# Kernel tuning notes

Hardware: AMD Instinct MI355X
Metric: run time of the kernel (lower is better)

The kernel has to match this reference:

```python
import jax, jax.numpy as jnp
import numpy as np

EPS = 1e-5
GROUPS = 32
K = 7  # correlation kernel size (min(7, 14))


def group_norm(x, w, b):
    B, C, H, W = x.shape
    xg = x.reshape(B, GROUPS, C // GROUPS, H, W)
    m = xg.mean(axis=(2, 3, 4), keepdims=True)
    v = xg.var(axis=(2, 3, 4), keepdims=True)
    xg = (xg - m) * jax.lax.rsqrt(v + EPS)
    return xg.reshape(B, C, H, W) * w[None, :, None, None] + b[None, :, None, None]


def conv1x1(x, w):  # w: [O, C]
    return jnp.einsum('bchw,oc->bohw', x, w)


def setup_inputs() -> dict:
    key = jax.random.key(0)
    ks = jax.random.split(key, 16)
    C, CC = 256, 64
    d = {}
    d['template_feat'] = jax.random.normal(ks[0], (32, C, 14, 14), jnp.float32)
    d['search_feat'] = jax.random.normal(ks[1], (32, C, 64, 64), jnp.float32)
    s1 = 1.0 / np.sqrt(C)
    d['w_t'] = jax.random.normal(ks[2], (CC, C), jnp.float32) * s1
    d['gn_t_w'] = jnp.ones((CC,), jnp.float32)
    d['gn_t_b'] = jnp.zeros((CC,), jnp.float32)
    d['w_s'] = jax.random.normal(ks[3], (CC, C), jnp.float32) * s1
    d['gn_s_w'] = jnp.ones((CC,), jnp.float32)
    d['gn_s_b'] = jnp.zeros((CC,), jnp.float32)
    d['w_p1'] = jax.random.normal(ks[4], (CC, CC, 3, 3), jnp.float32) * (1.0 / np.sqrt(CC * 9))
    d['gn_p_w'] = jnp.ones((CC,), jnp.float32)
    d['gn_p_b'] = jnp.zeros((CC,), jnp.float32)
    d['w_p2'] = jax.random.normal(ks[5], (1, CC), jnp.float32) * (1.0 / np.sqrt(CC))
    d['b_p2'] = jnp.zeros((1,), jnp.float32)
    return d


def reference(template_feat, search_feat, w_t, gn_t_w, gn_t_b, w_s, gn_s_w, gn_s_b,
              w_p1, gn_p_w, gn_p_b, w_p2, b_p2):
    B, _, Hs, Ws = search_feat.shape
    CC = w_t.shape[0]

    t = jax.nn.relu(group_norm(conv1x1(template_feat, w_t), gn_t_w, gn_t_b))   # [B,CC,14,14]
    s = jax.nn.relu(group_norm(conv1x1(search_feat, w_s), gn_s_w, gn_s_b))     # [B,CC,Hs,Ws]

    # global correlation: adaptive pool template to (1,1) == mean
    t_global = t.mean(axis=(2, 3), keepdims=True)
    global_corr = s * t_global

    # local depthwise correlation: adaptive pool 14x14 -> 7x7 (exact 2x2 mean)
    Ht = t.shape[2]
    r = Ht // K
    t_kernel = t.reshape(B, CC, K, r, K, r).mean(axis=(3, 5))                  # [B,CC,7,7]

    # batched per-sample depthwise conv: fold batch into groups
    x = s.reshape(1, B * CC, Hs, Ws)
    kern = t_kernel.reshape(B * CC, 1, K, K)
    local = jax.lax.conv_general_dilated(
        x, kern, window_strides=(1, 1), padding=[(K // 2, K // 2)] * 2,
        dimension_numbers=('NCHW', 'OIHW', 'NCHW'),
        feature_group_count=B * CC)
    local_corr = local.reshape(B, CC, Hs, Ws)

    corr = global_corr + local_corr

    # post_corr: 3x3 conv -> GN -> ReLU -> 1x1 conv (+bias)
    y = jax.lax.conv_general_dilated(
        corr, w_p1, window_strides=(1, 1), padding='SAME',
        dimension_numbers=('NCHW', 'OIHW', 'NCHW'))
    y = jax.nn.relu(group_norm(y, gn_p_w, gn_p_b))
    out = conv1x1(y, w_p2) + b_p2[None, :, None, None]                          # [B,1,Hs,Ws]
    return out
```

## Files before the change

### kernel.cpp

```cpp
#include <hip/hip_runtime.h>

#define EPS 1e-5f


typedef __attribute__((ext_vector_type(8))) short short8;
typedef __attribute__((ext_vector_type(4))) float floatx4;

__device__ __forceinline__ unsigned short f2bf(float x) {
    union { float f; unsigned u; } v; v.f = x;
    unsigned r = v.u + 0x7FFFu + ((v.u >> 16) & 1u);
    return (unsigned short)(r >> 16);
}
__device__ __forceinline__ float bf2f(unsigned short h) {
    union { unsigned u; float f; } v; v.u = ((unsigned)h) << 16;
    return v.f;
}

__global__ __launch_bounds__(256) void k1_template(
    const float* __restrict__ tmpl, const float* __restrict__ w_t,
    const float* __restrict__ gnw, const float* __restrict__ gnb,
    float* __restrict__ t_global, float* __restrict__ t_kernel)
{
    int b = blockIdx.x >> 2, h = blockIdx.x & 3;
    int tid = threadIdx.x;
    __shared__ float Xs[32][200];
    __shared__ float T[16][200];
    __shared__ float sums[16], sumsq[16], A[16], Bb[16];
    float acc[16];
    #pragma unroll
    for (int o = 0; o < 16; ++o) acc[o] = 0.f;
    const float* wb = w_t + (h * 16) * 256;
    const float* tb = tmpl + b * 50176;
    int p = tid;
    for (int chunk = 0; chunk < 8; ++chunk) {
        __syncthreads();
        #pragma unroll
        for (int j = 0; j < 7; ++j) {
            int f4 = tid + (j << 8);
            if (f4 < 1568) {
                int ic = f4 / 49, px4 = (f4 - ic * 49) << 2;
                float4 v = *(const float4*)(tb + (chunk * 32 + ic) * 196 + px4);
                *(float4*)&Xs[ic][px4] = v;
            }
        }
        __syncthreads();
        if (p < 196) {
            for (int cc = 0; cc < 32; ++cc) {
                float xv = Xs[cc][p];
                #pragma unroll
                for (int o = 0; o < 16; ++o)
                    acc[o] += xv * wb[o * 256 + chunk * 32 + cc];
            }
        }
    }
    __syncthreads();
    if (p < 196) {
        #pragma unroll
        for (int o = 0; o < 16; ++o) T[o][p] = acc[o];
    }
    __syncthreads();
    if (tid < 16) {
        float s = 0.f, s2 = 0.f;
        for (int q = 0; q < 196; ++q) { float v = T[tid][q]; s += v; s2 += v * v; }
        sums[tid] = s; sumsq[tid] = s2;
    }
    __syncthreads();
    if (tid < 8) {
        float S  = sums[2 * tid] + sums[2 * tid + 1];
        float S2 = sumsq[2 * tid] + sumsq[2 * tid + 1];
        float mean = S * (1.f / 392.f);
        float var  = S2 * (1.f / 392.f) - mean * mean;
        float inv  = rsqrtf(var + EPS);
        for (int e = 0; e < 2; ++e) {
            int c = 2 * tid + e, gc = h * 16 + c;
            float a = gnw[gc] * inv;
            A[c] = a; Bb[c] = gnb[gc] - mean * a;
        }
    }
    __syncthreads();
    if (p < 196) {
        #pragma unroll
        for (int o = 0; o < 16; ++o) {
            float v = A[o] * T[o][p] + Bb[o];
            T[o][p] = v > 0.f ? v : 0.f;
        }
    }
    __syncthreads();
    if (tid < 16) {
        int c = tid, gc = h * 16 + c;
        float s = 0.f;
        for (int q = 0; q < 196; ++q) s += T[c][q];
        t_global[b * 64 + gc] = s * (1.f / 196.f);
        for (int t = 0; t < 49; ++t) {
            int ky = t / 7, kx = t - 7 * ky;
            float v = T[c][(2 * ky) * 14 + 2 * kx]     + T[c][(2 * ky) * 14 + 2 * kx + 1]
                    + T[c][(2 * ky + 1) * 14 + 2 * kx] + T[c][(2 * ky + 1) * 14 + 2 * kx + 1];
            t_kernel[(b * 64 + gc) * 49 + t] = v * 0.25f;
        }
    }
}

__global__ __launch_bounds__(256) void k_w2(
    const float* __restrict__ w, unsigned short* __restrict__ wsb)
{
    int i = blockIdx.x * 256 + threadIdx.x;
    if (i < 16384) wsb[i] = f2bf(w[i]);
}

__global__ __launch_bounds__(256) void k2_mfma(
    const float* __restrict__ x, const unsigned short* __restrict__ wsb,
    float* __restrict__ sraw)
{
    int b = blockIdx.y, p0 = blockIdx.x << 8;
    int tid = threadIdx.x;
    int wave = tid >> 6, lane = tid & 63, q = lane >> 4, l15 = lane & 15;
    __shared__ short tile[256 * 64];

    floatx4 acc[4][4];
    #pragma unroll
    for (int i = 0; i < 4; ++i)
        #pragma unroll
        for (int mt = 0; mt < 4; ++mt) acc[i][mt] = (floatx4){0.f, 0.f, 0.f, 0.f};

    const float* xb = x + ((long)b << 20) + p0 + tid;
    for (int chunk = 0; chunk < 4; ++chunk) {
        __syncthreads();
        #pragma unroll
        for (int half = 0; half < 2; ++half) {
            float v[32];
            #pragma unroll
            for (int i = 0; i < 32; ++i)
                v[i] = xb[(long)((chunk << 6) + (half << 5) + i) << 12];
            #pragma unroll
            for (int blk = 0; blk < 4; ++blk) {
                int icblk = (half << 2) + blk;
                short8 s;
                #pragma unroll
                for (int e = 0; e < 8; ++e) s[e] = (short)f2bf(v[(blk << 3) + e]);
                int sw = icblk ^ (tid & 7);
                *(short8*)&tile[(tid << 6) + (sw << 3)] = s;
            }
        }
        __syncthreads();
        #pragma unroll
        for (int kq = 0; kq < 2; ++kq) {
            short8 afr[4], bfr[4];
            int kbase = (chunk << 6) + (kq << 5) + (q << 3);
            #pragma unroll
            for (int mt = 0; mt < 4; ++mt)
                afr[mt] = *(const short8*)(wsb + ((mt << 4) + l15) * 256 + kbase);
            #pragma unroll
            for (int i = 0; i < 4; ++i) {
                int px = (((wave << 2) + i) << 4) + l15;
                int sw = ((kq << 2) + q) ^ (px & 7);
                bfr[i] = *(const short8*)&tile[(px << 6) + (sw << 3)];
            }
            #pragma unroll
            for (int i = 0; i < 4; ++i)
                #pragma unroll
                for (int mt = 0; mt < 4; ++mt)
                    acc[i][mt] = __builtin_amdgcn_mfma_f32_16x16x32_bf16(afr[mt], bfr[i], acc[i][mt], 0, 0, 0);
        }
    }
    float* ob = sraw + ((long)b << 18) + p0;
    #pragma unroll
    for (int i = 0; i < 4; ++i) {
        int pxb = ((wave << 2) + i) << 4;
        #pragma unroll
        for (int mt = 0; mt < 4; ++mt)
            #pragma unroll
            for (int r = 0; r < 4; ++r) {
                int oc = (mt << 4) + (q << 2) + r;
                ob[(oc << 12) + pxb + l15] = acc[i][mt][r];
            }
    }
}

__global__ __launch_bounds__(256) void k_stats(
    const float* __restrict__ src, const float* __restrict__ gnw, const float* __restrict__ gnb,
    float* __restrict__ A, float* __restrict__ Bc)
{
    int g = blockIdx.x, b = blockIdx.y;
    int tid = threadIdx.x;
    const float* base = src + (((long)b * 64 + 2 * g) << 12);
    float s = 0.f, s2 = 0.f;
    for (int l = 0; l < 32; ++l) {
        float v = base[tid + (l << 8)];
        s += v; s2 += v * v;
    }
    #pragma unroll
    for (int off = 32; off > 0; off >>= 1) {
        s  += __shfl_down(s, off, 64);
        s2 += __shfl_down(s2, off, 64);
    }
    __shared__ float rs[4], rs2[4];
    int wid = tid >> 6, lane = tid & 63;
    if (lane == 0) { rs[wid] = s; rs2[wid] = s2; }
    __syncthreads();
    if (tid == 0) {
        float S = rs[0] + rs[1] + rs[2] + rs[3];
        float S2 = rs2[0] + rs2[1] + rs2[2] + rs2[3];
        float mean = S * (1.f / 8192.f);
        float var  = S2 * (1.f / 8192.f) - mean * mean;
        float inv  = rsqrtf(var + EPS);
        for (int e = 0; e < 2; ++e) {
            int c = 2 * g + e;
            float a = gnw[c] * inv;
            A[b * 64 + c] = a;
            Bc[b * 64 + c] = gnb[c] - mean * a;
        }
    }
}

__global__ __launch_bounds__(256) void k4_corr(
    const float* __restrict__ sraw, const float* __restrict__ A, const float* __restrict__ Bc,
    const float* __restrict__ t_global, const float* __restrict__ t_kernel,
    float* __restrict__ corr)
{
    int bc = blockIdx.x;
    int tid = threadIdx.x;
    __shared__ float tile[70 * 70];
    __shared__ float ker[49];
    float a = A[bc], bb = Bc[bc], tg = t_global[bc];
    for (int i = tid; i < 4900; i += 256) tile[i] = 0.f;
    if (tid < 49) ker[tid] = t_kernel[bc * 49 + tid];
    __syncthreads();
    const float* sb = sraw + ((long)bc << 12);
    for (int i = tid; i < 4096; i += 256) {
        int y = i >> 6, xx = i & 63;
        float v = a * sb[i] + bb;
        tile[(y + 3) * 70 + xx + 3] = v > 0.f ? v : 0.f;
    }
    __syncthreads();
    int x = tid & 63, ys = (tid >> 6) << 4;
    float acc[16];
    #pragma unroll
    for (int j = 0; j < 16; ++j) acc[j] = 0.f;
    #pragma unroll
    for (int kx = 0; kx < 7; ++kx) {
        float col[22];
        #pragma unroll
        for (int j = 0; j < 22; ++j) col[j] = tile[(ys + j) * 70 + x + kx];
        #pragma unroll
        for (int ky = 0; ky < 7; ++ky) {
            float kv = ker[ky * 7 + kx];
            #pragma unroll
            for (int j = 0; j < 16; ++j) acc[j] += kv * col[j + ky];
        }
    }
    float* ob = corr + ((long)bc << 12);
    #pragma unroll
    for (int j = 0; j < 16; ++j) {
        float sval = tile[(ys + j + 3) * 70 + x + 3];
        ob[((ys + j) << 6) + x] = acc[j] + sval * tg;
    }
}

__global__ __launch_bounds__(256) void k_t(
    const float* __restrict__ corr, unsigned short* __restrict__ corrT)
{
    int py = blockIdx.x, b = blockIdx.y;
    int tid = threadIdx.x;
    __shared__ float T[64][65];
    {
        int c0 = tid >> 6, px = tid & 63;
        const float* src = corr + (((long)b * 64) << 12) + (py << 6) + px;
        #pragma unroll
        for (int i = 0; i < 16; ++i) {
            int c = c0 + (i << 2);
            T[c][px] = src[(long)c << 12];
        }
    }
    __syncthreads();
    int ob = tid & 7, pxw = tid >> 3;
    unsigned short* dst = corrT + ((((b << 12)) + (py << 6)) << 6);
    #pragma unroll
    for (int i = 0; i < 2; ++i) {
        int p = pxw + (i << 5);
        unsigned w0 = (unsigned)f2bf(T[8 * ob + 0][p]) | ((unsigned)f2bf(T[8 * ob + 1][p]) << 16);
        unsigned w1 = (unsigned)f2bf(T[8 * ob + 2][p]) | ((unsigned)f2bf(T[8 * ob + 3][p]) << 16);
        unsigned w2 = (unsigned)f2bf(T[8 * ob + 4][p]) | ((unsigned)f2bf(T[8 * ob + 5][p]) << 16);
        unsigned w3 = (unsigned)f2bf(T[8 * ob + 6][p]) | ((unsigned)f2bf(T[8 * ob + 7][p]) << 16);
        uint4 val = {w0, w1, w2, w3};
        *(uint4*)(dst + ((long)p << 6) + (ob << 3)) = val;
    }
}

__global__ __launch_bounds__(256) void k_w(
    const float* __restrict__ w1, unsigned short* __restrict__ wpk)
{
    int i = blockIdx.x * 256 + threadIdx.x;
    if (i >= 36864) return;
    int c = i >> 11;
    int rem = i & 2047;
    int oc = rem >> 5;
    int k = rem & 31;
    int tap = c >> 1;
    int ic = ((c & 1) << 5) + k;
    wpk[i] = f2bf(w1[oc * 576 + ic * 9 + tap]);
}

__global__ __launch_bounds__(256) void k5_mfma(
    const unsigned short* __restrict__ corrT, const unsigned short* __restrict__ wpk,
    unsigned short* __restrict__ y)
{
    int b = blockIdx.y, py0 = blockIdx.x << 2;
    int tid = threadIdx.x;
    int wave = tid >> 6, lane = tid & 63, q = lane >> 4, l15 = lane & 15;
    __shared__ short tile[25344];

    for (int u = tid; u < 3168; u += 256) {
        int icblk = u & 7, rc = u >> 3;
        int row = rc / 66, col = rc - 66 * row;
        int py = py0 - 1 + row, px = col - 1;
        short8 v = {0, 0, 0, 0, 0, 0, 0, 0};
        if (py >= 0 && py < 64 && px >= 0 && px < 64)
            v = *(const short8*)(corrT + (((b << 12) + (py << 6) + px) << 6) + (icblk << 3));
        int sw = icblk ^ (col & 7);
        *(short8*)&tile[(rc << 6) + (sw << 3)] = v;
    }
    __syncthreads();

    floatx4 acc[4][4];
    #pragma unroll
    for (int i = 0; i < 4; ++i)
        #pragma unroll
        for (int ot = 0; ot < 4; ++ot) acc[i][ot] = (floatx4){0.f, 0.f, 0.f, 0.f};

    int pt0 = wave << 2;
    int rowb[4], colb[4];
    #pragma unroll
    for (int i = 0; i < 4; ++i) {
        int p = ((pt0 + i) << 4) + l15;
        rowb[i] = p >> 6;
        colb[i] = p & 63;
    }
    #pragma unroll
    for (int c = 0; c < 18; ++c) {
        const int tap = c >> 1, ky = tap / 3, kx = tap % 3, h = c & 1;
        short8 bfr[4], afr[4];
        #pragma unroll
        for (int ot = 0; ot < 4; ++ot)
            bfr[ot] = *(const short8*)(wpk + ((c << 6) + (ot << 4) + l15) * 32 + (q << 3));
        #pragma unroll
        for (int i = 0; i < 4; ++i) {
            int row = rowb[i] + ky, col = colb[i] + kx;
            int sw = ((h << 2) + q) ^ (col & 7);
            afr[i] = *(const short8*)&tile[((row * 66 + col) << 6) + (sw << 3)];
        }
        #pragma unroll
        for (int i = 0; i < 4; ++i)
            #pragma unroll
            for (int ot = 0; ot < 4; ++ot)
                acc[i][ot] = __builtin_amdgcn_mfma_f32_16x16x32_bf16(afr[i], bfr[ot], acc[i][ot], 0, 0, 0);
    }
    #pragma unroll
    for (int i = 0; i < 4; ++i) {
        #pragma unroll
        for (int r = 0; r < 4; ++r) {
            int p = ((pt0 + i) << 4) + (q << 2) + r;
            int py = py0 + (p >> 6), pxc = p & 63;
            int base = ((b << 12) + (py << 6) + pxc) << 6;
            #pragma unroll
            for (int ot = 0; ot < 4; ++ot)
                y[base + (ot << 4) + l15] = f2bf(acc[i][ot][r]);
        }
    }
}

__global__ __launch_bounds__(256) void k_sy1(
    const unsigned short* __restrict__ y, float* __restrict__ P1, float* __restrict__ P2)
{
    int sl = blockIdx.x, b = blockIdx.y;
    int tid = threadIdx.x;
    int ocp = tid & 31, px0 = tid >> 5;
    const unsigned* yp = (const unsigned*)y;
    float se = 0, s2e = 0, so = 0, s2o = 0;
    for (int k = 0; k < 64; ++k) {
        int px = (sl << 9) + (k << 3) + px0;
        unsigned u = yp[(((b << 12) + px) << 5) + ocp];
        float f0 = bf2f((unsigned short)(u & 0xFFFF));
        float f1 = bf2f((unsigned short)(u >> 16));
        se += f0; s2e += f0 * f0; so += f1; s2o += f1 * f1;
    }
    se += __shfl_down(se, 32, 64);  s2e += __shfl_down(s2e, 32, 64);
    so += __shfl_down(so, 32, 64);  s2o += __shfl_down(s2o, 32, 64);
    __shared__ float R[4][32][4];
    int w = tid >> 6, l = tid & 63;
    if (l < 32) { R[w][l][0] = se; R[w][l][1] = s2e; R[w][l][2] = so; R[w][l][3] = s2o; }
    __syncthreads();
    if (tid < 32) {
        float a0 = 0, a1 = 0, a2 = 0, a3 = 0;
        for (int w2 = 0; w2 < 4; ++w2) {
            a0 += R[w2][tid][0]; a1 += R[w2][tid][1]; a2 += R[w2][tid][2]; a3 += R[w2][tid][3];
        }
        int idx = ((b << 3) + sl) << 6;
        P1[idx + 2 * tid]     = a0; P2[idx + 2 * tid]     = a1;
        P1[idx + 2 * tid + 1] = a2; P2[idx + 2 * tid + 1] = a3;
    }
}

__global__ __launch_bounds__(64) void k_sy2(
    const float* __restrict__ P1, const float* __restrict__ P2,
    const float* __restrict__ gnw, const float* __restrict__ gnb,
    float* __restrict__ A, float* __restrict__ Bc)
{
    int b = blockIdx.x, c = threadIdx.x;
    float s = 0, s2 = 0;
    for (int sl = 0; sl < 8; ++sl) {
        int idx = (((b << 3) + sl) << 6) + c;
        s += P1[idx]; s2 += P2[idx];
    }
    float sp = __shfl_xor(s, 1, 64), s2p = __shfl_xor(s2, 1, 64);
    float S = s + sp, S2 = s2 + s2p;
    float mean = S * (1.f / 8192.f);
    float var  = S2 * (1.f / 8192.f) - mean * mean;
    float inv  = rsqrtf(var + EPS);
    float a = gnw[c] * inv;
    A[b * 64 + c] = a;
    Bc[b * 64 + c] = gnb[c] - mean * a;
}

__global__ __launch_bounds__(256) void k6_nhwc(
    const unsigned short* __restrict__ y, const float* __restrict__ A, const float* __restrict__ Bc,
    const float* __restrict__ w2, const float* __restrict__ b2, float* __restrict__ out)
{
    int b = blockIdx.y;
    int px0 = blockIdx.x << 9;
    int tid = threadIdx.x, wave = tid >> 6, lane = tid & 63;
    int ocp = lane & 31, ph = lane >> 5;
    int c0 = 2 * ocp;
    float a0 = A[b * 64 + c0],     b0 = Bc[b * 64 + c0],     w20 = w2[c0];
    float a1 = A[b * 64 + c0 + 1], b1 = Bc[b * 64 + c0 + 1], w21 = w2[c0 + 1];
    float bias = b2[0];
    const unsigned* yp = (const unsigned*)y;
    for (int i = 0; i < 64; ++i) {
        int px = px0 + (i << 3) + (wave << 1) + ph;
        unsigned u = yp[(((b << 12) + px) << 5) + ocp];
        float f0 = bf2f((unsigned short)(u & 0xFFFF));
        float f1 = bf2f((unsigned short)(u >> 16));
        float v0 = a0 * f0 + b0; v0 = v0 > 0.f ? v0 : 0.f;
        float v1 = a1 * f1 + b1; v1 = v1 > 0.f ? v1 : 0.f;
        float val = w20 * v0 + w21 * v1;
        #pragma unroll
        for (int m = 16; m >= 1; m >>= 1) val += __shfl_xor(val, m, 64);
        if (ocp == 0) out[(b << 12) + px] = val + bias;
    }
}

extern "C" void kernel_launch(void* const* d_in, const int* in_sizes, int n_in,
                              void* d_out, int out_size, void* d_ws, size_t ws_size,
                              hipStream_t stream)
{
    const float* tmpl   = (const float*)d_in[0];
    const float* search = (const float*)d_in[1];
    const float* w_t    = (const float*)d_in[2];
    const float* gn_t_w = (const float*)d_in[3];
    const float* gn_t_b = (const float*)d_in[4];
    const float* w_s    = (const float*)d_in[5];
    const float* gn_s_w = (const float*)d_in[6];
    const float* gn_s_b = (const float*)d_in[7];
    const float* w_p1   = (const float*)d_in[8];
    const float* gn_p_w = (const float*)d_in[9];
    const float* gn_p_b = (const float*)d_in[10];
    const float* w_p2   = (const float*)d_in[11];
    const float* b_p2   = (const float*)d_in[12];
    float* out = (float*)d_out;
    float* ws  = (float*)d_ws;

    float* TG   = ws;
    float* TK   = ws + 2048;
    float* AS   = ws + 102400;
    float* BS   = ws + 104448;
    float* AY   = ws + 106496;
    float* BY   = ws + 108544;
    float* P1   = ws + 110592;
    float* P2   = ws + 126976;
    unsigned short* WPK = (unsigned short*)(ws + 143360);
    float* SRAW = ws + 163840;
    float* CORR = ws + 163840 + 8388608;
    unsigned short* YRAW  = (unsigned short*)SRAW;
    unsigned short* CORRT = (unsigned short*)(SRAW + 4194304);
    unsigned short* WSB   = (unsigned short*)CORR;

    k_w2<<<64, 256, 0, stream>>>(w_s, WSB);
    k1_template<<<128, 256, 0, stream>>>(tmpl, w_t, gn_t_w, gn_t_b, TG, TK);
    k_w<<<144, 256, 0, stream>>>(w_p1, WPK);
    k2_mfma<<<dim3(16, 32), 256, 0, stream>>>(search, WSB, SRAW);
    k_stats<<<dim3(32, 32), 256, 0, stream>>>(SRAW, gn_s_w, gn_s_b, AS, BS);
    k4_corr<<<2048, 256, 0, stream>>>(SRAW, AS, BS, TG, TK, CORR);
    k_t<<<dim3(64, 32), 256, 0, stream>>>(CORR, CORRT);
    k5_mfma<<<dim3(16, 32), 256, 0, stream>>>(CORRT, WPK, YRAW);
    k_sy1<<<dim3(8, 32), 256, 0, stream>>>(YRAW, P1, P2);
    k_sy2<<<32, 64, 0, stream>>>(P1, P2, gn_p_w, gn_p_b, AY, BY);
    k6_nhwc<<<dim3(8, 32), 256, 0, stream>>>(YRAW, AY, BY, w_p2, b_p2, out);
}
```

Before: 361.4 us.

## Fuse GroupNorm stats into MFMA epilogues and compute correlation directly in NHWC bf16

The search 1x1-conv kernel now writes its output in NHWC and accumulates per-channel sum and sum-of-squares partials in its epilogue. This removes the separate stats pass over the 32 MB intermediate. The depthwise correlation kernel reads NHWC tiles with halos and writes bf16 NHWC directly, so the separate fp32 corr buffer and transpose kernel are gone. The 3x3-conv kernel likewise emits GroupNorm partials, replacing the two-kernel stats reduction. In exchange there is extra epilogue shuffling, and the halo tiles are reloaded redundantly in the correlation kernel.

```diff
diff --git a/kernel.cpp b/kernel.cpp
--- a/kernel.cpp
+++ b/kernel.cpp
@@ -107,185 +107,6 @@
     if (i < 16384) wsb[i] = f2bf(w[i]);
 }
 
-__global__ __launch_bounds__(256) void k2_mfma(
-    const float* __restrict__ x, const unsigned short* __restrict__ wsb,
-    float* __restrict__ sraw)
-{
-    int b = blockIdx.y, p0 = blockIdx.x << 8;
-    int tid = threadIdx.x;
-    int wave = tid >> 6, lane = tid & 63, q = lane >> 4, l15 = lane & 15;
-    __shared__ short tile[256 * 64];
-
-    floatx4 acc[4][4];
-    #pragma unroll
-    for (int i = 0; i < 4; ++i)
-        #pragma unroll
-        for (int mt = 0; mt < 4; ++mt) acc[i][mt] = (floatx4){0.f, 0.f, 0.f, 0.f};
-
-    const float* xb = x + ((long)b << 20) + p0 + tid;
-    for (int chunk = 0; chunk < 4; ++chunk) {
-        __syncthreads();
-        #pragma unroll
-        for (int half = 0; half < 2; ++half) {
-            float v[32];
-            #pragma unroll
-            for (int i = 0; i < 32; ++i)
-                v[i] = xb[(long)((chunk << 6) + (half << 5) + i) << 12];
-            #pragma unroll
-            for (int blk = 0; blk < 4; ++blk) {
-                int icblk = (half << 2) + blk;
-                short8 s;
-                #pragma unroll
-                for (int e = 0; e < 8; ++e) s[e] = (short)f2bf(v[(blk << 3) + e]);
-                int sw = icblk ^ (tid & 7);
-                *(short8*)&tile[(tid << 6) + (sw << 3)] = s;
-            }
-        }
-        __syncthreads();
-        #pragma unroll
-        for (int kq = 0; kq < 2; ++kq) {
-            short8 afr[4], bfr[4];
-            int kbase = (chunk << 6) + (kq << 5) + (q << 3);
-            #pragma unroll
-            for (int mt = 0; mt < 4; ++mt)
-                afr[mt] = *(const short8*)(wsb + ((mt << 4) + l15) * 256 + kbase);
-            #pragma unroll
-            for (int i = 0; i < 4; ++i) {
-                int px = (((wave << 2) + i) << 4) + l15;
-                int sw = ((kq << 2) + q) ^ (px & 7);
-                bfr[i] = *(const short8*)&tile[(px << 6) + (sw << 3)];
-            }
-            #pragma unroll
-            for (int i = 0; i < 4; ++i)
-                #pragma unroll
-                for (int mt = 0; mt < 4; ++mt)
-                    acc[i][mt] = __builtin_amdgcn_mfma_f32_16x16x32_bf16(afr[mt], bfr[i], acc[i][mt], 0, 0, 0);
-        }
-    }
-    float* ob = sraw + ((long)b << 18) + p0;
-    #pragma unroll
-    for (int i = 0; i < 4; ++i) {
-        int pxb = ((wave << 2) + i) << 4;
-        #pragma unroll
-        for (int mt = 0; mt < 4; ++mt)
-            #pragma unroll
-            for (int r = 0; r < 4; ++r) {
-                int oc = (mt << 4) + (q << 2) + r;
-                ob[(oc << 12) + pxb + l15] = acc[i][mt][r];
-            }
-    }
-}
-
-__global__ __launch_bounds__(256) void k_stats(
-    const float* __restrict__ src, const float* __restrict__ gnw, const float* __restrict__ gnb,
-    float* __restrict__ A, float* __restrict__ Bc)
-{
-    int g = blockIdx.x, b = blockIdx.y;
-    int tid = threadIdx.x;
-    const float* base = src + (((long)b * 64 + 2 * g) << 12);
-    float s = 0.f, s2 = 0.f;
-    for (int l = 0; l < 32; ++l) {
-        float v = base[tid + (l << 8)];
-        s += v; s2 += v * v;
-    }
-    #pragma unroll
-    for (int off = 32; off > 0; off >>= 1) {
-        s  += __shfl_down(s, off, 64);
-        s2 += __shfl_down(s2, off, 64);
-    }
-    __shared__ float rs[4], rs2[4];
-    int wid = tid >> 6, lane = tid & 63;
-    if (lane == 0) { rs[wid] = s; rs2[wid] = s2; }
-    __syncthreads();
-    if (tid == 0) {
-        float S = rs[0] + rs[1] + rs[2] + rs[3];
-        float S2 = rs2[0] + rs2[1] + rs2[2] + rs2[3];
-        float mean = S * (1.f / 8192.f);
-        float var  = S2 * (1.f / 8192.f) - mean * mean;
-        float inv  = rsqrtf(var + EPS);
-        for (int e = 0; e < 2; ++e) {
-            int c = 2 * g + e;
-            float a = gnw[c] * inv;
-            A[b * 64 + c] = a;
-            Bc[b * 64 + c] = gnb[c] - mean * a;
-        }
-    }
-}
-
-__global__ __launch_bounds__(256) void k4_corr(
-    const float* __restrict__ sraw, const float* __restrict__ A, const float* __restrict__ Bc,
-    const float* __restrict__ t_global, const float* __restrict__ t_kernel,
-    float* __restrict__ corr)
-{
-    int bc = blockIdx.x;
-    int tid = threadIdx.x;
-    __shared__ float tile[70 * 70];
-    __shared__ float ker[49];
-    float a = A[bc], bb = Bc[bc], tg = t_global[bc];
-    for (int i = tid; i < 4900; i += 256) tile[i] = 0.f;
-    if (tid < 49) ker[tid] = t_kernel[bc * 49 + tid];
-    __syncthreads();
-    const float* sb = sraw + ((long)bc << 12);
-    for (int i = tid; i < 4096; i += 256) {
-        int y = i >> 6, xx = i & 63;
-        float v = a * sb[i] + bb;
-        tile[(y + 3) * 70 + xx + 3] = v > 0.f ? v : 0.f;
-    }
-    __syncthreads();
-    int x = tid & 63, ys = (tid >> 6) << 4;
-    float acc[16];
-    #pragma unroll
-    for (int j = 0; j < 16; ++j) acc[j] = 0.f;
-    #pragma unroll
-    for (int kx = 0; kx < 7; ++kx) {
-        float col[22];
-        #pragma unroll
-        for (int j = 0; j < 22; ++j) col[j] = tile[(ys + j) * 70 + x + kx];
-        #pragma unroll
-        for (int ky = 0; ky < 7; ++ky) {
-            float kv = ker[ky * 7 + kx];
-            #pragma unroll
-            for (int j = 0; j < 16; ++j) acc[j] += kv * col[j + ky];
-        }
-    }
-    float* ob = corr + ((long)bc << 12);
-    #pragma unroll
-    for (int j = 0; j < 16; ++j) {
-        float sval = tile[(ys + j + 3) * 70 + x + 3];
-        ob[((ys + j) << 6) + x] = acc[j] + sval * tg;
-    }
-}
-
-__global__ __launch_bounds__(256) void k_t(
-    const float* __restrict__ corr, unsigned short* __restrict__ corrT)
-{
-    int py = blockIdx.x, b = blockIdx.y;
-    int tid = threadIdx.x;
-    __shared__ float T[64][65];
-    {
-        int c0 = tid >> 6, px = tid & 63;
-        const float* src = corr + (((long)b * 64) << 12) + (py << 6) + px;
-        #pragma unroll
-        for (int i = 0; i < 16; ++i) {
-            int c = c0 + (i << 2);
-            T[c][px] = src[(long)c << 12];
-        }
-    }
-    __syncthreads();
-    int ob = tid & 7, pxw = tid >> 3;
-    unsigned short* dst = corrT + ((((b << 12)) + (py << 6)) << 6);
-    #pragma unroll
-    for (int i = 0; i < 2; ++i) {
-        int p = pxw + (i << 5);
-        unsigned w0 = (unsigned)f2bf(T[8 * ob + 0][p]) | ((unsigned)f2bf(T[8 * ob + 1][p]) << 16);
-        unsigned w1 = (unsigned)f2bf(T[8 * ob + 2][p]) | ((unsigned)f2bf(T[8 * ob + 3][p]) << 16);
-        unsigned w2 = (unsigned)f2bf(T[8 * ob + 4][p]) | ((unsigned)f2bf(T[8 * ob + 5][p]) << 16);
-        unsigned w3 = (unsigned)f2bf(T[8 * ob + 6][p]) | ((unsigned)f2bf(T[8 * ob + 7][p]) << 16);
-        uint4 val = {w0, w1, w2, w3};
-        *(uint4*)(dst + ((long)p << 6) + (ob << 3)) = val;
-    }
-}
-
 __global__ __launch_bounds__(256) void k_w(
     const float* __restrict__ w1, unsigned short* __restrict__ wpk)
 {
@@ -300,14 +121,194 @@
     wpk[i] = f2bf(w1[oc * 576 + ic * 9 + tap]);
 }
 
+__global__ __launch_bounds__(256) void k2_mfma(
+    const float* __restrict__ x, const unsigned short* __restrict__ wsb,
+    float* __restrict__ s_nhwc, float* __restrict__ Psum, float* __restrict__ Psq)
+{
+    int b = blockIdx.y, p0 = blockIdx.x << 8;
+    int tid = threadIdx.x;
+    int wave = tid >> 6, lane = tid & 63, q = lane >> 4, l15 = lane & 15;
+    __shared__ short tile[256 * 64];
+    __shared__ float RED[4][64][2];
+
+    floatx4 acc[4][4];
+    #pragma unroll
+    for (int i = 0; i < 4; ++i)
+        #pragma unroll
+        for (int mt = 0; mt < 4; ++mt) acc[i][mt] = (floatx4){0.f, 0.f, 0.f, 0.f};
+
+    const float* xb = x + ((long)b << 20) + p0 + tid;
+    for (int chunk = 0; chunk < 4; ++chunk) {
+        __syncthreads();
+        #pragma unroll
+        for (int half = 0; half < 2; ++half) {
+            float v[32];
+            #pragma unroll
+            for (int i = 0; i < 32; ++i)
+                v[i] = xb[(long)((chunk << 6) + (half << 5) + i) << 12];
+            #pragma unroll
+            for (int blk = 0; blk < 4; ++blk) {
+                int icblk = (half << 2) + blk;
+                short8 s;
+                #pragma unroll
+                for (int e = 0; e < 8; ++e) s[e] = (short)f2bf(v[(blk << 3) + e]);
+                int sw = icblk ^ (tid & 7);
+                *(short8*)&tile[(tid << 6) + (sw << 3)] = s;
+            }
+        }
+        __syncthreads();
+        #pragma unroll
+        for (int kq = 0; kq < 2; ++kq) {
+            short8 afr[4], bfr[4];
+            int kbase = (chunk << 6) + (kq << 5) + (q << 3);
+            #pragma unroll
+            for (int mt = 0; mt < 4; ++mt)
+                afr[mt] = *(const short8*)(wsb + ((mt << 4) + l15) * 256 + kbase);
+            #pragma unroll
+            for (int i = 0; i < 4; ++i) {
+                int px = (((wave << 2) + i) << 4) + l15;
+                int sw = ((kq << 2) + q) ^ (px & 7);
+                bfr[i] = *(const short8*)&tile[(px << 6) + (sw << 3)];
+            }
+            #pragma unroll
+            for (int i = 0; i < 4; ++i)
+                #pragma unroll
+                for (int mt = 0; mt < 4; ++mt)
+                    acc[i][mt] = __builtin_amdgcn_mfma_f32_16x16x32_bf16(afr[mt], bfr[i], acc[i][mt], 0, 0, 0);
+        }
+    }
+    #pragma unroll
+    for (int mt = 0; mt < 4; ++mt)
+        #pragma unroll
+        for (int r = 0; r < 4; ++r) {
+            float sv = 0.f, qv = 0.f;
+            #pragma unroll
+            for (int i = 0; i < 4; ++i) { float v = acc[i][mt][r]; sv += v; qv += v * v; }
+            #pragma unroll
+            for (int m = 1; m <= 8; m <<= 1) {
+                sv += __shfl_xor(sv, m, 64);
+                qv += __shfl_xor(qv, m, 64);
+            }
+            if (l15 == 0) {
+                RED[wave][(mt << 4) + (q << 2) + r][0] = sv;
+                RED[wave][(mt << 4) + (q << 2) + r][1] = qv;
+            }
+        }
+    float* ob = s_nhwc + ((long)b << 18) + ((long)p0 << 6);
+    #pragma unroll
+    for (int i = 0; i < 4; ++i) {
+        int px = (((wave << 2) + i) << 4) + l15;
+        #pragma unroll
+        for (int mt = 0; mt < 4; ++mt)
+            *(floatx4*)(ob + (px << 6) + (mt << 4) + (q << 2)) = acc[i][mt];
+    }
+    __syncthreads();
+    if (tid < 64) {
+        float S = 0.f, Q = 0.f;
+        #pragma unroll
+        for (int w = 0; w < 4; ++w) { S += RED[w][tid][0]; Q += RED[w][tid][1]; }
+        int idx = (((blockIdx.x << 5) + b) << 6) + tid;
+        Psum[idx] = S; Psq[idx] = Q;
+    }
+}
+
+__global__ __launch_bounds__(64) void k_fin(
+    const float* __restrict__ Ps, const float* __restrict__ Pq,
+    const float* __restrict__ gnw, const float* __restrict__ gnb,
+    float* __restrict__ A, float* __restrict__ Bc)
+{
+    int b = blockIdx.x, c = threadIdx.x;
+    float s = 0.f, s2 = 0.f;
+    for (int k = 0; k < 16; ++k) {
+        int idx = (((k << 5) + b) << 6) + c;
+        s += Ps[idx]; s2 += Pq[idx];
+    }
+    float sp = __shfl_xor(s, 1, 64), qp = __shfl_xor(s2, 1, 64);
+    float S = s + sp, Q = s2 + qp;
+    float mean = S * (1.f / 8192.f);
+    float var  = Q * (1.f / 8192.f) - mean * mean;
+    float inv  = rsqrtf(var + EPS);
+    float a = gnw[c] * inv;
+    A[b * 64 + c] = a;
+    Bc[b * 64 + c] = gnb[c] - mean * a;
+}
+
+__global__ __launch_bounds__(256) void k4_nhwc(
+    const float* __restrict__ s_nhwc, const float* __restrict__ A, const float* __restrict__ Bc,
+    const float* __restrict__ t_global, const float* __restrict__ t_kernel,
+    unsigned short* __restrict__ corrT)
+{
+    int bx = blockIdx.x & 7, by = blockIdx.x >> 3, b = blockIdx.y;
+    int px0 = bx << 3, py0 = by << 3;
+    int tid = threadIdx.x, c = tid & 63, slot = tid >> 6;
+    __shared__ float H[14 * 14 * 64];
+    const float* sb = s_nhwc + ((long)b << 18);
+    int ch4 = tid & 15;
+    float4 a4 = *(const float4*)(A  + b * 64 + (ch4 << 2));
+    float4 b4 = *(const float4*)(Bc + b * 64 + (ch4 << 2));
+    for (int f4 = tid; f4 < 3136; f4 += 256) {
+        int cell = f4 >> 4;
+        int r = cell / 14, c2 = cell - 14 * r;
+        int gy = py0 - 3 + r, gx = px0 - 3 + c2;
+        float4 v = {0.f, 0.f, 0.f, 0.f};
+        if (gy >= 0 && gy < 64 && gx >= 0 && gx < 64) {
+            float4 rv = *(const float4*)(sb + (((gy << 6) + gx) << 6) + (ch4 << 2));
+            v.x = a4.x * rv.x + b4.x; v.x = v.x > 0.f ? v.x : 0.f;
+            v.y = a4.y * rv.y + b4.y; v.y = v.y > 0.f ? v.y : 0.f;
+            v.z = a4.z * rv.z + b4.z; v.z = v.z > 0.f ? v.z : 0.f;
+            v.w = a4.w * rv.w + b4.w; v.w = v.w > 0.f ? v.w : 0.f;
+        }
+        *(float4*)&H[(cell << 6) + (ch4 << 2)] = v;
+    }
+    float tg = t_global[b * 64 + c];
+    float kreg[49];
+    #pragma unroll
+    for (int t = 0; t < 49; ++t) kreg[t] = t_kernel[(b * 64 + c) * 49 + t];
+    __syncthreads();
+    int oy = slot << 1;
+    float win[7][8];
+    #pragma unroll
+    for (int kx = 0; kx < 7; ++kx)
+        #pragma unroll
+        for (int j = 0; j < 8; ++j)
+            win[kx][j] = H[(((oy + j) * 14 + kx) << 6) + c];
+    unsigned short* ob = corrT + ((long)b << 18);
+    #pragma unroll
+    for (int ox = 0; ox < 8; ++ox) {
+        if (ox > 0) {
+            int sl = (ox + 6) % 7;
+            #pragma unroll
+            for (int j = 0; j < 8; ++j)
+                win[sl][j] = H[(((oy + j) * 14 + ox + 6) << 6) + c];
+        }
+        float a0 = 0.f, a1 = 0.f;
+        #pragma unroll
+        for (int kx = 0; kx < 7; ++kx) {
+            int sl = (ox + kx) % 7;
+            #pragma unroll
+            for (int ky = 0; ky < 7; ++ky) {
+                float kv = kreg[ky * 7 + kx];
+                a0 += kv * win[sl][ky];
+                a1 += kv * win[sl][ky + 1];
+            }
+        }
+        int cs = (ox + 3) % 7;
+        a0 += win[cs][3] * tg;
+        a1 += win[cs][4] * tg;
+        ob[((((py0 + oy) << 6) + px0 + ox) << 6) + c]     = f2bf(a0);
+        ob[((((py0 + oy + 1) << 6) + px0 + ox) << 6) + c] = f2bf(a1);
+    }
+}
+
 __global__ __launch_bounds__(256) void k5_mfma(
     const unsigned short* __restrict__ corrT, const unsigned short* __restrict__ wpk,
-    unsigned short* __restrict__ y)
+    unsigned short* __restrict__ y, float* __restrict__ Psum, float* __restrict__ Psq)
 {
     int b = blockIdx.y, py0 = blockIdx.x << 2;
     int tid = threadIdx.x;
     int wave = tid >> 6, lane = tid & 63, q = lane >> 4, l15 = lane & 15;
     __shared__ short tile[25344];
+    __shared__ float RED[4][64][2];
 
     for (int u = tid; u < 3168; u += 256) {
         int icblk = u & 7, rc = u >> 3;
@@ -355,6 +356,17 @@
                 acc[i][ot] = __builtin_amdgcn_mfma_f32_16x16x32_bf16(afr[i], bfr[ot], acc[i][ot], 0, 0, 0);
     }
     #pragma unroll
+    for (int ot = 0; ot < 4; ++ot) {
+        float sv = 0.f, qv = 0.f;
+        #pragma unroll
+        for (int i = 0; i < 4; ++i)
+            #pragma unroll
+            for (int r = 0; r < 4; ++r) { float v = acc[i][ot][r]; sv += v; qv += v * v; }
+        sv += __shfl_xor(sv, 16, 64); qv += __shfl_xor(qv, 16, 64);
+        sv += __shfl_xor(sv, 32, 64); qv += __shfl_xor(qv, 32, 64);
+        if (q == 0) { RED[wave][(ot << 4) + l15][0] = sv; RED[wave][(ot << 4) + l15][1] = qv; }
+    }
+    #pragma unroll
     for (int i = 0; i < 4; ++i) {
         #pragma unroll
         for (int r = 0; r < 4; ++r) {
@@ -366,59 +378,14 @@
                 y[base + (ot << 4) + l15] = f2bf(acc[i][ot][r]);
         }
     }
-}
-
-__global__ __launch_bounds__(256) void k_sy1(
-    const unsigned short* __restrict__ y, float* __restrict__ P1, float* __restrict__ P2)
-{
-    int sl = blockIdx.x, b = blockIdx.y;
-    int tid = threadIdx.x;
-    int ocp = tid & 31, px0 = tid >> 5;
-    const unsigned* yp = (const unsigned*)y;
-    float se = 0, s2e = 0, so = 0, s2o = 0;
-    for (int k = 0; k < 64; ++k) {
-        int px = (sl << 9) + (k << 3) + px0;
-        unsigned u = yp[(((b << 12) + px) << 5) + ocp];
-        float f0 = bf2f((unsigned short)(u & 0xFFFF));
-        float f1 = bf2f((unsigned short)(u >> 16));
-        se += f0; s2e += f0 * f0; so += f1; s2o += f1 * f1;
-    }
-    se += __shfl_down(se, 32, 64);  s2e += __shfl_down(s2e, 32, 64);
-    so += __shfl_down(so, 32, 64);  s2o += __shfl_down(s2o, 32, 64);
-    __shared__ float R[4][32][4];
-    int w = tid >> 6, l = tid & 63;
-    if (l < 32) { R[w][l][0] = se; R[w][l][1] = s2e; R[w][l][2] = so; R[w][l][3] = s2o; }
-    __syncthreads();
-    if (tid < 32) {
-        float a0 = 0, a1 = 0, a2 = 0, a3 = 0;
-        for (int w2 = 0; w2 < 4; ++w2) {
-            a0 += R[w2][tid][0]; a1 += R[w2][tid][1]; a2 += R[w2][tid][2]; a3 += R[w2][tid][3];
-        }
-        int idx = ((b << 3) + sl) << 6;
-        P1[idx + 2 * tid]     = a0; P2[idx + 2 * tid]     = a1;
-        P1[idx + 2 * tid + 1] = a2; P2[idx + 2 * tid + 1] = a3;
-    }
-}
-
-__global__ __launch_bounds__(64) void k_sy2(
-    const float* __restrict__ P1, const float* __restrict__ P2,
-    const float* __restrict__ gnw, const float* __restrict__ gnb,
-    float* __restrict__ A, float* __restrict__ Bc)
-{
-    int b = blockIdx.x, c = threadIdx.x;
-    float s = 0, s2 = 0;
-    for (int sl = 0; sl < 8; ++sl) {
-        int idx = (((b << 3) + sl) << 6) + c;
-        s += P1[idx]; s2 += P2[idx];
-    }
-    float sp = __shfl_xor(s, 1, 64), s2p = __shfl_xor(s2, 1, 64);
-    float S = s + sp, S2 = s2 + s2p;
-    float mean = S * (1.f / 8192.f);
-    float var  = S2 * (1.f / 8192.f) - mean * mean;
-    float inv  = rsqrtf(var + EPS);
-    float a = gnw[c] * inv;
-    A[b * 64 + c] = a;
-    Bc[b * 64 + c] = gnb[c] - mean * a;
+    __syncthreads();
+    if (tid < 64) {
+        float S = 0.f, Q = 0.f;
+        #pragma unroll
+        for (int w = 0; w < 4; ++w) { S += RED[w][tid][0]; Q += RED[w][tid][1]; }
+        int idx = (((blockIdx.x << 5) + b) << 6) + tid;
+        Psum[idx] = S; Psq[idx] = Q;
+    }
 }
 
 __global__ __launch_bounds__(256) void k6_nhwc(
@@ -474,24 +441,21 @@
     float* BS   = ws + 104448;
     float* AY   = ws + 106496;
     float* BY   = ws + 108544;
-    float* P1   = ws + 110592;
-    float* P2   = ws + 126976;
-    unsigned short* WPK = (unsigned short*)(ws + 143360);
-    float* SRAW = ws + 163840;
-    float* CORR = ws + 163840 + 8388608;
-    unsigned short* YRAW  = (unsigned short*)SRAW;
-    unsigned short* CORRT = (unsigned short*)(SRAW + 4194304);
-    unsigned short* WSB   = (unsigned short*)CORR;
+    float* PS   = ws + 110592;
+    float* PQ   = ws + 143360;
+    unsigned short* WPK = (unsigned short*)(ws + 176128);
+    unsigned short* WSB = (unsigned short*)(ws + 194560);
+    float* SN = ws + 202752;
+    unsigned short* CORRT = (unsigned short*)(ws + 202752 + 8388608);
+    unsigned short* YRAW  = (unsigned short*)(ws + 202752 + 12582912);
 
     k_w2<<<64, 256, 0, stream>>>(w_s, WSB);
+    k_w<<<144, 256, 0, stream>>>(w_p1, WPK);
     k1_template<<<128, 256, 0, stream>>>(tmpl, w_t, gn_t_w, gn_t_b, TG, TK);
-    k_w<<<144, 256, 0, stream>>>(w_p1, WPK);
-    k2_mfma<<<dim3(16, 32), 256, 0, stream>>>(search, WSB, SRAW);
-    k_stats<<<dim3(32, 32), 256, 0, stream>>>(SRAW, gn_s_w, gn_s_b, AS, BS);
-    k4_corr<<<2048, 256, 0, stream>>>(SRAW, AS, BS, TG, TK, CORR);
-    k_t<<<dim3(64, 32), 256, 0, stream>>>(CORR, CORRT);
-    k5_mfma<<<dim3(16, 32), 256, 0, stream>>>(CORRT, WPK, YRAW);
-    k_sy1<<<dim3(8, 32), 256, 0, stream>>>(YRAW, P1, P2);
-    k_sy2<<<32, 64, 0, stream>>>(P1, P2, gn_p_w, gn_p_b, AY, BY);
+    k2_mfma<<<dim3(16, 32), 256, 0, stream>>>(search, WSB, SN, PS, PQ);
+    k_fin<<<32, 64, 0, stream>>>(PS, PQ, gn_s_w, gn_s_b, AS, BS);
+    k4_nhwc<<<dim3(64, 32), 256, 0, stream>>>(SN, AS, BS, TG, TK, CORRT);
+    k5_mfma<<<dim3(16, 32), 256, 0, stream>>>(CORRT, WPK, YRAW, PS, PQ);
+    k_fin<<<32, 64, 0, stream>>>(PS, PQ, gn_p_w, gn_p_b, AY, BY);
     k6_nhwc<<<dim3(8, 32), 256, 0, stream>>>(YRAW, AY, BY, w_p2, b_p2, out);
 }
```

Measured after the change: 361.4 us. No clear change (+0.0%).
